# Kernel optimization log

Measured on AMD Instinct MI355X. Metric: run time of the kernel, lower is better.

## Reference

```python
import jax, jax.numpy as jnp
import numpy as np

N_AGENTS = 2
B, C, H, W = 4, 64, 200, 352


def _conv(x, w, b):
    # x: (n, Cin, H, W), w: (Cout, Cin, 3, 3), 'SAME' padding, stride 1
    y = jax.lax.conv_general_dilated(
        x, w, window_strides=(1, 1), padding='SAME',
        dimension_numbers=('NCHW', 'OIHW', 'NCHW'))
    return y + b[None, :, None, None]


def setup_inputs() -> dict:
    key = jax.random.key(0)
    ks = jax.random.split(key, 4)
    s = 0.05  # small init so sigmoid/tanh stay in useful range
    x = jax.random.normal(ks[0], (N_AGENTS, B, C, H, W), dtype=jnp.float32)
    msg_w = jax.random.normal(ks[1], (C, 2 * C, 3, 3), dtype=jnp.float32) * s
    msg_b = jnp.zeros((C,), jnp.float32)
    gates_w = jax.random.normal(ks[2], (2 * C, 3 * C, 3, 3), dtype=jnp.float32) * s
    gates_b = jnp.zeros((2 * C,), jnp.float32)
    can_w = jax.random.normal(ks[3], (C, 3 * C, 3, 3), dtype=jnp.float32) * s
    can_b = jnp.zeros((C,), jnp.float32)
    return {'x': x, 'msg_w': msg_w, 'msg_b': msg_b,
            'gates_w': gates_w, 'gates_b': gates_b,
            'can_w': can_w, 'can_b': can_b}


def reference(x, msg_w, msg_b, gates_w, gates_b, can_w, can_b):
    # num_iteration=1; only new_x[0] (agent 0's updated feature) is returned,
    # so we compute exactly that path.
    x0, x1 = x[0], x[1]                       # each (B, C, H, W)
    neighbor = jnp.concatenate([x0, x1], axis=1)   # (B, 2C, H, W)
    message = _conv(neighbor, msg_w, msg_b)        # (B, C, H, W)
    agg = 0.5 * (x0 + message)                     # 'avg' over stacked pair
    cat_feat = jnp.concatenate([x0, agg], axis=1)  # (B, 2C, H, W)

    # ConvGRU: batch_first input (1, B, 2C, H, W) -> sequence length B, batch 1
    h0 = jnp.zeros((1, C, H, W), cat_feat.dtype)

    def step(h, inp):
        inp = inp[None]                                     # (1, 2C, H, W)
        comb = jnp.concatenate([inp, h], axis=1)            # (1, 3C, H, W)
        gates = jax.nn.sigmoid(_conv(comb, gates_w, gates_b))
        reset, update = jnp.split(gates, 2, axis=1)         # each (1, C, H, W)
        comb2 = jnp.concatenate([inp, reset * h], axis=1)
        cnm = jnp.tanh(_conv(comb2, can_w, can_b))
        h_next = (1.0 - update) * h + update * cnm
        return h_next, h_next[0]

    _, out = jax.lax.scan(step, h0, cat_feat)  # out: (B, C, H, W)
    return out
```

## Files before the change

### kernel.cpp

```cpp
#include <hip/hip_runtime.h>
#include <math.h>
#include <string.h>

#define HH 200
#define WW 352
#define HWSZ (HH*WW)
#define CHW (64L*HWSZ)

enum { EPI_MSG=0, EPI_GATES=1, EPI_CAND=2 };

typedef __attribute__((ext_vector_type(8))) _Float16 f16x8;
typedef __attribute__((ext_vector_type(4))) float f32x4;
typedef __attribute__((ext_vector_type(4))) unsigned int uint4v;
typedef __attribute__((ext_vector_type(4))) unsigned short ushort4v;

__device__ __forceinline__ unsigned short f2h(float f) {
    _Float16 h = (_Float16)f;
    return __builtin_bit_cast(unsigned short, h);
}
__device__ __forceinline__ float h2f(unsigned short u) {
    return (float)__builtin_bit_cast(_Float16, u);
}

__device__ __forceinline__ void load_lds16(const unsigned short* g,
                                           unsigned short* l) {
    __builtin_amdgcn_global_load_lds(
        (const __attribute__((address_space(1))) unsigned int*)g,
        (__attribute__((address_space(3))) unsigned int*)l, 16, 0, 0);
}

__global__ void prepack_k(const float* __restrict__ mw,
                          const float* __restrict__ gw,
                          const float* __restrict__ cw,
                          unsigned short* __restrict__ pw,
                          unsigned short* __restrict__ zp)
{
    const int MSG_I = 4*18432;
    const int GAT_I = 12*18432;
    const int CAN_I = 6*18432;
    const int TOTAL = MSG_I + GAT_I + CAN_I;
    int idx = blockIdx.x*256 + threadIdx.x;
    if (idx >= TOTAL) {
        int r = idx - TOTAL;
        if (r < 128) zp[r] = 0;
        return;
    }
    const float* w; int cin, nkb, rel; unsigned short* base;
    if (idx < MSG_I)              { w=mw; cin=128; nkb=4; rel=idx;              base=pw; }
    else if (idx < MSG_I+GAT_I)   { w=gw; cin=192; nkb=6; rel=idx-MSG_I;        base=pw+73728; }
    else                          { w=cw; cin=192; nkb=6; rel=idx-MSG_I-GAT_I;  base=pw+294912; }
    int chunk = rel / 18432, r = rel - chunk*18432;
    int j = r & 7, lane = (r >> 3) & 63, cfsh = r >> 9;
    int cf = cfsh & 3, sh = cfsh >> 2;
    int q = lane >> 4, n16 = lane & 15;
    int co_l = cf*16 + n16, ch = q*8 + j;
    int cogrp = chunk / nkb, kb = chunk - cogrp*nkb;
    float f = w[(((long)(cogrp*64 + co_l))*cin + kb*32 + ch)*9 + sh];
    base[(size_t)chunk*18432 + r] = f2h(f);
}

__global__ void convert_all_k(const float* __restrict__ x,
                              unsigned short* __restrict__ xb0_all,
                              unsigned short* __restrict__ xb1_all)
{
    int idx = blockIdx.x*256 + threadIdx.x;
    int cp   = idx & 15;
    int rest = idx >> 4;
    int px4  = rest % 17600;
    int r2   = rest / 17600;
    int hb = r2 & 1, ag = (r2 >> 1) & 1, t = r2 >> 2;
    const float* src = x + ((size_t)(ag*4 + t))*CHW
                         + (size_t)(hb*32 + 2*cp)*HWSZ + (size_t)px4*4;
    float4 a = *(const float4*)src;
    float4 b = *(const float4*)(src + HWSZ);
    unsigned int* dst = (unsigned int*)((ag ? xb1_all : xb0_all)
                        + (size_t)t*CHW + (size_t)hb*HWSZ*32) + (size_t)px4*64 + cp;
    dst[0]  = (unsigned)f2h(a.x) | ((unsigned)f2h(b.x) << 16);
    dst[16] = (unsigned)f2h(a.y) | ((unsigned)f2h(b.y) << 16);
    dst[32] = (unsigned)f2h(a.z) | ((unsigned)f2h(b.z) << 16);
    dst[48] = (unsigned)f2h(a.w) | ((unsigned)f2h(b.w) << 16);
}

template<int EPI>
__global__ __launch_bounds__(256, 2)
void conv_mfma_k(const unsigned short* __restrict__ seg0b,
                 const unsigned short* __restrict__ seg1b,
                 const unsigned short* __restrict__ seg2b,
                 int nkb, int nkb_stride, int grp_base,
                 const unsigned short* __restrict__ pw,
                 const unsigned short* __restrict__ zp,
                 const float* __restrict__ bias,
                 const unsigned short* e_hb,
                 const unsigned short* __restrict__ e_updb,
                 float* out_f,
                 unsigned short* out_b,
                 unsigned short* out_b2)
{
    __shared__ unsigned short s_in0[340*32];
    __shared__ unsigned short s_in1[340*32];
    __shared__ unsigned short s_w[9*4*64*8];

    const int tid  = threadIdx.x;
    const int lane = tid & 63;
    const int wv   = tid >> 6;
    const int n16  = lane & 15;
    const int q    = lane >> 4;

    const int z = blockIdx.z;
    int grp, ts = 0;
    if (EPI == EPI_MSG) { ts = z; grp = 0; } else grp = z + grp_base;

    const unsigned short* s0 = seg0b + (EPI==EPI_MSG ? (size_t)ts*CHW : 0);
    const unsigned short* s1 = seg1b + (EPI==EPI_MSG ? (size_t)ts*CHW : 0);
    unsigned short* ob = out_b;
    if (EPI == EPI_MSG) ob = (ts < 3) ? out_b + (size_t)ts*CHW : out_b2;

    const int x0p = blockIdx.x * 32;
    const int y0  = blockIdx.y * 8;

    int hdst0 = 0, hdst1 = 0; size_t hsrc0 = 0, hsrc1 = 0;
    bool hval0 = false, hval1 = false;
    {
        auto hcalc = [&](int s, int& hdst, size_t& hsrc, bool& hval) {
            int hp = s >> 2, gs = s & 3;
            int row, col;
            if (hp < 34)      { row = 0; col = hp; }
            else if (hp < 68) { row = 9; col = hp - 34; }
            else { int k = hp - 68; row = 1 + (k >> 1); col = (k & 1) * 33; }
            int pos = row*34 + col;
            int gy = y0 + row - 1, gx = x0p + col - 1;
            hdst = (pos << 5) + (gs << 3);
            int g = (gs ^ pos ^ (pos >> 2)) & 3;
            if ((unsigned)gy < (unsigned)HH && (unsigned)gx < (unsigned)WW) {
                hval = true;
                hsrc = ((size_t)(gy*WW + gx) << 5) + (size_t)(g << 3);
            }
        };
        if (tid < 336) hcalc(tid, hdst0, hsrc0, hval0);
        if (tid < 80)  hcalc(tid + 256, hdst1, hsrc1, hval1);
    }

    auto srcof = [&](int kb) -> const unsigned short* {
        return ((kb < 2) ? s0 : (kb < 4) ? s1 : seg2b) + (size_t)(kb & 1)*HWSZ*32;
    };

    struct HV { uint4v a, b; };
    auto halo_load = [&](int kb, HV& h) {
        const unsigned short* src = srcof(kb);
        if (tid < 336) h.a = *(const uint4v*)(hval0 ? src + hsrc0 : zp);
        if (tid < 80)  h.b = *(const uint4v*)(hval1 ? src + hsrc1 : zp);
    };
    auto halo_write = [&](unsigned short* bin, const HV& h) {
        if (tid < 336) *(uint4v*)&bin[hdst0] = h.a;
        if (tid < 80)  *(uint4v*)&bin[hdst1] = h.b;
    };

    auto stage_in = [&](int kb, unsigned short* bin) {
        const unsigned short* src = srcof(kb);
#pragma unroll
        for (int j = 0; j < 4; ++j) {
            const int c    = wv + 4*j;
            const int row  = 1 + (c >> 1);
            const int colh = c & 1;
            const int gy   = y0 + row - 1;
            const int p0   = row*34 + 1 + colh*16;
            const int pl   = p0 + (lane >> 2);
            const int g    = ((lane & 3) ^ pl ^ (pl >> 2)) & 3;
            const int gx   = x0p + colh*16 + (lane >> 2);
            load_lds16(src + (((size_t)(gy*WW + gx)) << 5) + (g << 3),
                       &bin[(size_t)p0 << 5]);
        }
    };
    auto stage_w = [&](int kb) {
        const unsigned short* wsrc = pw + (size_t)(grp*nkb_stride + kb)*18432;
#pragma unroll
        for (int i = 0; i < 9; ++i) {
            const int u = wv + 4*i;
            load_lds16(wsrc + (size_t)u*512 + (size_t)lane*8, &s_w[(size_t)u*512]);
        }
    };

    f32x4 acc[4][4];
#pragma unroll
    for (int cf=0; cf<4; ++cf)
#pragma unroll
        for (int p=0; p<4; ++p) acc[cf][p] = (f32x4){0.f,0.f,0.f,0.f};

    auto compute = [&](const unsigned short* sin) {
#pragma unroll
        for (int ky = 0; ky < 3; ++ky) {
#pragma unroll
            for (int kx = 0; kx < 3; ++kx) {
                const int sh = ky*3 + kx;
                f16x8 aw[4];
#pragma unroll
                for (int cf = 0; cf < 4; ++cf)
                    aw[cf] = *(const f16x8*)&s_w[((sh*4 + cf)*64 + lane)*8];
#pragma unroll
                for (int p = 0; p < 4; ++p) {
                    const int rl = 2*wv + (p >> 1) + ky;
                    const int cl = 16*(p & 1) + n16 + kx;
                    const int pos = rl*34 + cl;
                    const int sw = (q ^ pos ^ (pos >> 2)) & 3;
                    f16x8 bfr = *(const f16x8*)&sin[(pos << 5) + (sw << 3)];
#pragma unroll
                    for (int cf = 0; cf < 4; ++cf)
                        acc[cf][p] = __builtin_amdgcn_mfma_f32_16x16x32_f16(
                                         aw[cf], bfr, acc[cf][p], 0, 0, 0);
                }
            }
        }
    };

    HV h0, h1;
    stage_in(0, s_in0);
    stage_w(0);
    halo_load(0, h0);

    for (int kb = 0; kb < nkb; kb += 2) {
        halo_write(s_in0, h0);
        __syncthreads();
        halo_load(kb + 1, h1);
        stage_in(kb + 1, s_in1);
        __builtin_amdgcn_sched_barrier(0);
        compute(s_in0);
        __syncthreads();
        stage_w(kb + 1);
        halo_write(s_in1, h1);
        __syncthreads();
        if (kb + 2 < nkb) {
            halo_load(kb + 2, h0);
            stage_in(kb + 2, s_in0);
            __builtin_amdgcn_sched_barrier(0);
        }
        compute(s_in1);
        __syncthreads();
        if (kb + 2 < nkb) stage_w(kb + 2);
    }

#pragma unroll
    for (int cf = 0; cf < 4; ++cf) {
        const int half   = cf >> 1;
        const int cobase = grp*64 + cf*16 + q*4;
        const int cmod   = (cf & 1)*16 + q*4;
#pragma unroll
        for (int p = 0; p < 4; ++p) {
            const int row = y0 + 2*wv + (p >> 1);
            const int col = x0p + 16*(p & 1) + n16;
            if (row >= HH) continue;
            const long pix = (long)row*WW + col;
            const size_t iidx = (((size_t)half*HWSZ + pix) << 5) + cmod;
            float v[4];
#pragma unroll
            for (int r = 0; r < 4; ++r) v[r] = acc[cf][p][r] + bias[cobase + r];

            if (EPI == EPI_MSG) {
                ushort4v xv = *(const ushort4v*)&s0[iidx];
                ushort4v s;
#pragma unroll
                for (int r = 0; r < 4; ++r)
                    s[r] = f2h(0.5f*(h2f(xv[r]) + v[r]));
                *(ushort4v*)&ob[iidx] = s;
            } else if (EPI == EPI_GATES) {
                if (grp == 0) {
                    ushort4v hv = e_hb ? *(const ushort4v*)&e_hb[iidx]
                                       : (ushort4v){0,0,0,0};
                    ushort4v s;
#pragma unroll
                    for (int r = 0; r < 4; ++r) {
                        float g = 1.f/(1.f + __expf(-v[r]));
                        s[r] = f2h(g * h2f(hv[r]));
                    }
                    *(ushort4v*)&out_b[iidx] = s;
                } else {
                    ushort4v s;
#pragma unroll
                    for (int r = 0; r < 4; ++r)
                        s[r] = f2h(1.f/(1.f + __expf(-v[r])));
                    *(ushort4v*)&out_b2[iidx] = s;
                }
            } else {
                ushort4v uv = *(const ushort4v*)&e_updb[iidx];
                ushort4v hv = e_hb ? *(const ushort4v*)&e_hb[iidx]
                                   : (ushort4v){0,0,0,0};
                ushort4v s;
#pragma unroll
                for (int r = 0; r < 4; ++r) {
                    float cnm = tanhf(v[r]);
                    float u   = h2f(uv[r]);
                    float hn  = (1.f - u)*h2f(hv[r]) + u*cnm;
                    out_f[(long)(cobase+r)*HWSZ + pix] = hn;
                    s[r] = f2h(hn);
                }
                *(ushort4v*)&out_b[iidx] = s;
            }
        }
    }
}

extern "C" void kernel_launch(void* const* d_in, const int* in_sizes, int n_in,
                              void* d_out, int out_size, void* d_ws, size_t ws_size,
                              hipStream_t stream)
{
    const float* x       = (const float*)d_in[0];
    const float* msg_w   = (const float*)d_in[1];
    const float* msg_b   = (const float*)d_in[2];
    const float* gates_w = (const float*)d_in[3];
    const float* gates_b = (const float*)d_in[4];
    const float* can_w   = (const float*)d_in[5];
    const float* can_b   = (const float*)d_in[6];
    float* out = (float*)d_out;

    unsigned short* W       = (unsigned short*)d_ws;
    unsigned short* xb0_all = W;
    unsigned short* aggb3   = W + 4*CHW;
    unsigned short* rhb     = W + 5*CHW;
    unsigned short* updb    = W + 6*CHW;
    unsigned short* hb      = W + 7*CHW;
    unsigned short* pw      = W + 8*CHW;
    unsigned short* pw_msg  = pw;
    unsigned short* pw_gat  = pw + 73728;
    unsigned short* pw_can  = pw + 294912;
    unsigned short* zp      = pw + 405504;

    unsigned short* outU16   = (unsigned short*)d_out;
    unsigned short* xb1_all  = outU16;
    unsigned short* aggbase  = outU16 + 4*CHW;

    prepack_k<<<dim3(1585), dim3(256), 0, stream>>>(msg_w, gates_w, can_w, pw, zp);
    convert_all_k<<<dim3(17600), dim3(256), 0, stream>>>(x, xb0_all, xb1_all);

    conv_mfma_k<EPI_MSG><<<dim3(11,25,4), dim3(256), 0, stream>>>(
        xb0_all, xb1_all, nullptr, 4, 4, 0, pw_msg, zp, msg_b,
        nullptr, nullptr, nullptr, aggbase, aggb3);

    for (int t = 0; t < 4; ++t) {
        const unsigned short* xt  = xb0_all + (size_t)t*CHW;
        const unsigned short* agt = (t < 3) ? aggbase + (size_t)t*CHW : aggb3;
        const unsigned short* hprev = t ? hb : nullptr;

        conv_mfma_k<EPI_GATES><<<dim3(11,25, t ? 2 : 1), dim3(256), 0, stream>>>(
            xt, agt, hb, t ? 6 : 4, 6, t ? 0 : 1, pw_gat, zp, gates_b,
            hprev, nullptr, nullptr, rhb, updb);
        conv_mfma_k<EPI_CAND><<<dim3(11,25,1), dim3(256), 0, stream>>>(
            xt, agt, rhb, t ? 6 : 4, 6, 0, pw_can, zp, can_b,
            hprev, updb, out + (size_t)t*CHW, hb, nullptr);
    }
}
```

Before: 428.4 us.

## Split candidate and first-step gate convs into 32-channel blocks with double-buffered weights

Adds a CF template parameter so a block can compute 32 output channels instead of 64. The candidate conv and the t=0 update-gate conv now launch twice as many blocks, which fills more CUs for these single-group launches that previously ran only 275 blocks. The CF=2 path double-buffers weight tiles in LDS, removing the weight-restage barrier. The cost is that each input tile is staged twice across channel groups, and the extra prepacked gate weights are stored in scratch space inside the output buffer.

```diff
diff --git a/kernel.cpp b/kernel.cpp
--- a/kernel.cpp
+++ b/kernel.cpp
@@ -33,30 +33,40 @@
                           const float* __restrict__ gw,
                           const float* __restrict__ cw,
                           unsigned short* __restrict__ pw,
+                          unsigned short* __restrict__ gatu,
                           unsigned short* __restrict__ zp)
 {
-    const int MSG_I = 4*18432;
-    const int GAT_I = 12*18432;
-    const int CAN_I = 6*18432;
-    const int TOTAL = MSG_I + GAT_I + CAN_I;
+    const int MSG_I  = 4*18432;
+    const int GAT_I  = 12*18432;
+    const int CAN_I  = 12*9216;
+    const int GATU_I = 12*9216;
+    const int TOTAL  = MSG_I + GAT_I + CAN_I + GATU_I;
     int idx = blockIdx.x*256 + threadIdx.x;
     if (idx >= TOTAL) {
         int r = idx - TOTAL;
         if (r < 128) zp[r] = 0;
         return;
     }
-    const float* w; int cin, nkb, rel; unsigned short* base;
-    if (idx < MSG_I)              { w=mw; cin=128; nkb=4; rel=idx;              base=pw; }
-    else if (idx < MSG_I+GAT_I)   { w=gw; cin=192; nkb=6; rel=idx-MSG_I;        base=pw+73728; }
-    else                          { w=cw; cin=192; nkb=6; rel=idx-MSG_I-GAT_I;  base=pw+294912; }
-    int chunk = rel / 18432, r = rel - chunk*18432;
+    const float* w; int cin, nkb, CF, co_off, rel; unsigned short* base;
+    if (idx < MSG_I) {
+        w=mw; cin=128; nkb=4; CF=4; co_off=0;  rel=idx;                    base=pw;
+    } else if (idx < MSG_I+GAT_I) {
+        w=gw; cin=192; nkb=6; CF=4; co_off=0;  rel=idx-MSG_I;              base=pw+73728;
+    } else if (idx < MSG_I+GAT_I+CAN_I) {
+        w=cw; cin=192; nkb=6; CF=2; co_off=0;  rel=idx-MSG_I-GAT_I;        base=pw+294912;
+    } else {
+        w=gw; cin=192; nkb=6; CF=2; co_off=64; rel=idx-MSG_I-GAT_I-CAN_I;  base=gatu;
+    }
+    int per = CF*4608;
+    int chunk = rel / per, r = rel - chunk*per;
     int j = r & 7, lane = (r >> 3) & 63, cfsh = r >> 9;
-    int cf = cfsh & 3, sh = cfsh >> 2;
+    int cf = cfsh & (CF-1), sh = cfsh / CF;
     int q = lane >> 4, n16 = lane & 15;
     int co_l = cf*16 + n16, ch = q*8 + j;
     int cogrp = chunk / nkb, kb = chunk - cogrp*nkb;
-    float f = w[(((long)(cogrp*64 + co_l))*cin + kb*32 + ch)*9 + sh];
-    base[(size_t)chunk*18432 + r] = f2h(f);
+    int co = co_off + cogrp*(CF*16) + co_l;
+    float f = w[(((long)co)*cin + kb*32 + ch)*9 + sh];
+    base[(size_t)chunk*per + r] = f2h(f);
 }
 
 __global__ void convert_all_k(const float* __restrict__ x,
@@ -81,12 +91,12 @@
     dst[48] = (unsigned)f2h(a.w) | ((unsigned)f2h(b.w) << 16);
 }
 
-template<int EPI>
+template<int EPI, int CF>
 __global__ __launch_bounds__(256, 2)
 void conv_mfma_k(const unsigned short* __restrict__ seg0b,
                  const unsigned short* __restrict__ seg1b,
                  const unsigned short* __restrict__ seg2b,
-                 int nkb, int nkb_stride, int grp_base,
+                 int nkb, int nkb_stride, int co_off,
                  const unsigned short* __restrict__ pw,
                  const unsigned short* __restrict__ zp,
                  const float* __restrict__ bias,
@@ -98,7 +108,7 @@
 {
     __shared__ unsigned short s_in0[340*32];
     __shared__ unsigned short s_in1[340*32];
-    __shared__ unsigned short s_w[9*4*64*8];
+    __shared__ unsigned short s_w[18432];
 
     const int tid  = threadIdx.x;
     const int lane = tid & 63;
@@ -108,7 +118,7 @@
 
     const int z = blockIdx.z;
     int grp, ts = 0;
-    if (EPI == EPI_MSG) { ts = z; grp = 0; } else grp = z + grp_base;
+    if (EPI == EPI_MSG) { ts = z; grp = 0; } else grp = z;
 
     const unsigned short* s0 = seg0b + (EPI==EPI_MSG ? (size_t)ts*CHW : 0);
     const unsigned short* s1 = seg1b + (EPI==EPI_MSG ? (size_t)ts*CHW : 0);
@@ -171,31 +181,33 @@
                        &bin[(size_t)p0 << 5]);
         }
     };
-    auto stage_w = [&](int kb) {
-        const unsigned short* wsrc = pw + (size_t)(grp*nkb_stride + kb)*18432;
-#pragma unroll
-        for (int i = 0; i < 9; ++i) {
+    auto stage_w = [&](int kb, unsigned short* bw) {
+        const unsigned short* wsrc = pw + (size_t)(grp*nkb_stride + kb)*(CF*4608);
+        constexpr int NCH = (CF == 4) ? 36 : 18;
+#pragma unroll
+        for (int i = 0; i < (NCH + 3) / 4; ++i) {
             const int u = wv + 4*i;
-            load_lds16(wsrc + (size_t)u*512 + (size_t)lane*8, &s_w[(size_t)u*512]);
-        }
-    };
-
-    f32x4 acc[4][4];
-#pragma unroll
-    for (int cf=0; cf<4; ++cf)
+            if (u < NCH)
+                load_lds16(wsrc + (size_t)u*512 + (size_t)lane*8, &bw[(size_t)u*512]);
+        }
+    };
+
+    f32x4 acc[CF][4];
+#pragma unroll
+    for (int cf=0; cf<CF; ++cf)
 #pragma unroll
         for (int p=0; p<4; ++p) acc[cf][p] = (f32x4){0.f,0.f,0.f,0.f};
 
-    auto compute = [&](const unsigned short* sin) {
+    auto compute = [&](const unsigned short* sin, const unsigned short* swt) {
 #pragma unroll
         for (int ky = 0; ky < 3; ++ky) {
 #pragma unroll
             for (int kx = 0; kx < 3; ++kx) {
                 const int sh = ky*3 + kx;
-                f16x8 aw[4];
-#pragma unroll
-                for (int cf = 0; cf < 4; ++cf)
-                    aw[cf] = *(const f16x8*)&s_w[((sh*4 + cf)*64 + lane)*8];
+                f16x8 aw[CF];
+#pragma unroll
+                for (int cf = 0; cf < CF; ++cf)
+                    aw[cf] = *(const f16x8*)&swt[((sh*CF + cf)*64 + lane)*8];
 #pragma unroll
                 for (int p = 0; p < 4; ++p) {
                     const int rl = 2*wv + (p >> 1) + ky;
@@ -204,7 +216,7 @@
                     const int sw = (q ^ pos ^ (pos >> 2)) & 3;
                     f16x8 bfr = *(const f16x8*)&sin[(pos << 5) + (sw << 3)];
 #pragma unroll
-                    for (int cf = 0; cf < 4; ++cf)
+                    for (int cf = 0; cf < CF; ++cf)
                         acc[cf][p] = __builtin_amdgcn_mfma_f32_16x16x32_f16(
                                          aw[cf], bfr, acc[cf][p], 0, 0, 0);
                 }
@@ -213,36 +225,55 @@
     };
 
     HV h0, h1;
-    stage_in(0, s_in0);
-    stage_w(0);
-    halo_load(0, h0);
-
-    for (int kb = 0; kb < nkb; kb += 2) {
-        halo_write(s_in0, h0);
-        __syncthreads();
-        halo_load(kb + 1, h1);
-        stage_in(kb + 1, s_in1);
-        __builtin_amdgcn_sched_barrier(0);
-        compute(s_in0);
-        __syncthreads();
-        stage_w(kb + 1);
-        halo_write(s_in1, h1);
-        __syncthreads();
-        if (kb + 2 < nkb) {
-            halo_load(kb + 2, h0);
-            stage_in(kb + 2, s_in0);
+    if constexpr (CF == 4) {
+        stage_in(0, s_in0);
+        stage_w(0, s_w);
+        halo_load(0, h0);
+        for (int kb = 0; kb < nkb; kb += 2) {
+            halo_write(s_in0, h0);
+            __syncthreads();
+            halo_load(kb + 1, h1);
+            stage_in(kb + 1, s_in1);
             __builtin_amdgcn_sched_barrier(0);
-        }
-        compute(s_in1);
-        __syncthreads();
-        if (kb + 2 < nkb) stage_w(kb + 2);
-    }
-
-#pragma unroll
-    for (int cf = 0; cf < 4; ++cf) {
-        const int half   = cf >> 1;
-        const int cobase = grp*64 + cf*16 + q*4;
-        const int cmod   = (cf & 1)*16 + q*4;
+            compute(s_in0, s_w);
+            __syncthreads();
+            stage_w(kb + 1, s_w);
+            halo_write(s_in1, h1);
+            __syncthreads();
+            if (kb + 2 < nkb) {
+                halo_load(kb + 2, h0);
+                stage_in(kb + 2, s_in0);
+                __builtin_amdgcn_sched_barrier(0);
+            }
+            compute(s_in1, s_w);
+            __syncthreads();
+            if (kb + 2 < nkb) stage_w(kb + 2, s_w);
+        }
+    } else {
+        unsigned short* s_w0 = s_w;
+        unsigned short* s_w1 = s_w + 9216;
+        stage_in(0, s_in0); stage_w(0, s_w0); halo_load(0, h0);
+        for (int kb = 0; kb < nkb; kb += 2) {
+            halo_write(s_in0, h0);
+            __syncthreads();
+            stage_in(kb + 1, s_in1); stage_w(kb + 1, s_w1); halo_load(kb + 1, h1);
+            __builtin_amdgcn_sched_barrier(0);
+            compute(s_in0, s_w0);
+            halo_write(s_in1, h1);
+            __syncthreads();
+            if (kb + 2 < nkb) {
+                stage_in(kb + 2, s_in0); stage_w(kb + 2, s_w0); halo_load(kb + 2, h0);
+                __builtin_amdgcn_sched_barrier(0);
+            }
+            compute(s_in1, s_w1);
+        }
+    }
+
+#pragma unroll
+    for (int cf = 0; cf < CF; ++cf) {
+        const int co_r0 = co_off + grp*(CF*16) + cf*16 + q*4;
+        const int half  = (co_r0 >> 5) & 1;
+        const int cmod  = co_r0 & 31;
 #pragma unroll
         for (int p = 0; p < 4; ++p) {
             const int row = y0 + 2*wv + (p >> 1);
@@ -252,7 +283,7 @@
             const size_t iidx = (((size_t)half*HWSZ + pix) << 5) + cmod;
             float v[4];
 #pragma unroll
-            for (int r = 0; r < 4; ++r) v[r] = acc[cf][p][r] + bias[cobase + r];
+            for (int r = 0; r < 4; ++r) v[r] = acc[cf][p][r] + bias[co_r0 + r];
 
             if (EPI == EPI_MSG) {
                 ushort4v xv = *(const ushort4v*)&s0[iidx];
@@ -262,7 +293,7 @@
                     s[r] = f2h(0.5f*(h2f(xv[r]) + v[r]));
                 *(ushort4v*)&ob[iidx] = s;
             } else if (EPI == EPI_GATES) {
-                if (grp == 0) {
+                if (co_r0 < 64) {
                     ushort4v hv = e_hb ? *(const ushort4v*)&e_hb[iidx]
                                        : (ushort4v){0,0,0,0};
                     ushort4v s;
@@ -273,11 +304,13 @@
                     }
                     *(ushort4v*)&out_b[iidx] = s;
                 } else {
+                    const int cu = co_r0 - 64;
+                    const size_t uidx = (((size_t)(cu >> 5)*HWSZ + pix) << 5) + (cu & 31);
                     ushort4v s;
 #pragma unroll
                     for (int r = 0; r < 4; ++r)
                         s[r] = f2h(1.f/(1.f + __expf(-v[r])));
-                    *(ushort4v*)&out_b2[iidx] = s;
+                    *(ushort4v*)&out_b2[uidx] = s;
                 }
             } else {
                 ushort4v uv = *(const ushort4v*)&e_updb[iidx];
@@ -289,7 +322,7 @@
                     float cnm = tanhf(v[r]);
                     float u   = h2f(uv[r]);
                     float hn  = (1.f - u)*h2f(hv[r]) + u*cnm;
-                    out_f[(long)(cobase+r)*HWSZ + pix] = hn;
+                    out_f[(long)(co_r0 + r)*HWSZ + pix] = hn;
                     s[r] = f2h(hn);
                 }
                 *(ushort4v*)&out_b[iidx] = s;
@@ -326,11 +359,13 @@
     unsigned short* outU16   = (unsigned short*)d_out;
     unsigned short* xb1_all  = outU16;
     unsigned short* aggbase  = outU16 + 4*CHW;
-
-    prepack_k<<<dim3(1585), dim3(256), 0, stream>>>(msg_w, gates_w, can_w, pw, zp);
+    unsigned short* pw_gatu  = outU16 + 7*CHW;
+
+    prepack_k<<<dim3(2017), dim3(256), 0, stream>>>(msg_w, gates_w, can_w,
+                                                    pw, pw_gatu, zp);
     convert_all_k<<<dim3(17600), dim3(256), 0, stream>>>(x, xb0_all, xb1_all);
 
-    conv_mfma_k<EPI_MSG><<<dim3(11,25,4), dim3(256), 0, stream>>>(
+    conv_mfma_k<EPI_MSG,4><<<dim3(11,25,4), dim3(256), 0, stream>>>(
         xb0_all, xb1_all, nullptr, 4, 4, 0, pw_msg, zp, msg_b,
         nullptr, nullptr, nullptr, aggbase, aggb3);
 
@@ -339,10 +374,16 @@
         const unsigned short* agt = (t < 3) ? aggbase + (size_t)t*CHW : aggb3;
         const unsigned short* hprev = t ? hb : nullptr;
 
-        conv_mfma_k<EPI_GATES><<<dim3(11,25, t ? 2 : 1), dim3(256), 0, stream>>>(
-            xt, agt, hb, t ? 6 : 4, 6, t ? 0 : 1, pw_gat, zp, gates_b,
-            hprev, nullptr, nullptr, rhb, updb);
-        conv_mfma_k<EPI_CAND><<<dim3(11,25,1), dim3(256), 0, stream>>>(
+        if (t == 0) {
+            conv_mfma_k<EPI_GATES,2><<<dim3(11,25,2), dim3(256), 0, stream>>>(
+                xt, agt, nullptr, 4, 6, 64, pw_gatu, zp, gates_b,
+                nullptr, nullptr, nullptr, rhb, updb);
+        } else {
+            conv_mfma_k<EPI_GATES,4><<<dim3(11,25,2), dim3(256), 0, stream>>>(
+                xt, agt, hb, 6, 6, 0, pw_gat, zp, gates_b,
+                hprev, nullptr, nullptr, rhb, updb);
+        }
+        conv_mfma_k<EPI_CAND,2><<<dim3(11,25,2), dim3(256), 0, stream>>>(
             xt, agt, rhb, t ? 6 : 4, 6, 0, pw_can, zp, can_b,
             hprev, updb, out + (size_t)t*CHW, hb, nullptr);
     }
```

Result: slower. 441.5 us (+3.0%).

## Split conv blocks into 32-output-channel halves with single-buffered LDS for occupancy

Applied to the files above, without the earlier changes.

Each conv block now computes 32 output channels instead of 64, so the grid doubles along x and the accumulator and weight tiles shrink by half. LDS input double-buffering is dropped for a single buffer with a simpler load/compute/sync loop, and launch bounds rise to allow four blocks per CU. The weight prepack layout is rewritten to match 32-channel groups. The trade-off is that each input tile is now staged twice (once per channel half), and the software pipelining that overlapped loads with MFMA work is lost in exchange for more resident waves.

```diff
diff --git a/kernel.cpp b/kernel.cpp
--- a/kernel.cpp
+++ b/kernel.cpp
@@ -35,9 +35,9 @@
                           unsigned short* __restrict__ pw,
                           unsigned short* __restrict__ zp)
 {
-    const int MSG_I = 4*18432;
-    const int GAT_I = 12*18432;
-    const int CAN_I = 6*18432;
+    const int MSG_I = 8*9216;
+    const int GAT_I = 24*9216;
+    const int CAN_I = 12*9216;
     const int TOTAL = MSG_I + GAT_I + CAN_I;
     int idx = blockIdx.x*256 + threadIdx.x;
     if (idx >= TOTAL) {
@@ -46,17 +46,17 @@
         return;
     }
     const float* w; int cin, nkb, rel; unsigned short* base;
-    if (idx < MSG_I)              { w=mw; cin=128; nkb=4; rel=idx;              base=pw; }
-    else if (idx < MSG_I+GAT_I)   { w=gw; cin=192; nkb=6; rel=idx-MSG_I;        base=pw+73728; }
-    else                          { w=cw; cin=192; nkb=6; rel=idx-MSG_I-GAT_I;  base=pw+294912; }
-    int chunk = rel / 18432, r = rel - chunk*18432;
+    if (idx < MSG_I)              { w=mw; cin=128; nkb=4; rel=idx;             base=pw; }
+    else if (idx < MSG_I+GAT_I)   { w=gw; cin=192; nkb=6; rel=idx-MSG_I;       base=pw+73728; }
+    else                          { w=cw; cin=192; nkb=6; rel=idx-MSG_I-GAT_I; base=pw+294912; }
+    int chunk = rel / 9216, r = rel - chunk*9216;
     int j = r & 7, lane = (r >> 3) & 63, cfsh = r >> 9;
-    int cf = cfsh & 3, sh = cfsh >> 2;
+    int cf = cfsh & 1, sh = cfsh >> 1;
     int q = lane >> 4, n16 = lane & 15;
     int co_l = cf*16 + n16, ch = q*8 + j;
     int cogrp = chunk / nkb, kb = chunk - cogrp*nkb;
-    float f = w[(((long)(cogrp*64 + co_l))*cin + kb*32 + ch)*9 + sh];
-    base[(size_t)chunk*18432 + r] = f2h(f);
+    float f = w[(((long)(cogrp*32 + co_l))*cin + kb*32 + ch)*9 + sh];
+    base[(size_t)chunk*9216 + r] = f2h(f);
 }
 
 __global__ void convert_all_k(const float* __restrict__ x,
@@ -82,7 +82,7 @@
 }
 
 template<int EPI>
-__global__ __launch_bounds__(256, 2)
+__global__ __launch_bounds__(256, 4)
 void conv_mfma_k(const unsigned short* __restrict__ seg0b,
                  const unsigned short* __restrict__ seg1b,
                  const unsigned short* __restrict__ seg2b,
@@ -96,9 +96,8 @@
                  unsigned short* out_b,
                  unsigned short* out_b2)
 {
-    __shared__ unsigned short s_in0[340*32];
-    __shared__ unsigned short s_in1[340*32];
-    __shared__ unsigned short s_w[9*4*64*8];
+    __shared__ unsigned short s_in[340*32];
+    __shared__ unsigned short s_w[9*2*64*8];
 
     const int tid  = threadIdx.x;
     const int lane = tid & 63;
@@ -106,16 +105,16 @@
     const int n16  = lane & 15;
     const int q    = lane >> 4;
 
-    const int z = blockIdx.z;
     int grp, ts = 0;
-    if (EPI == EPI_MSG) { ts = z; grp = 0; } else grp = z + grp_base;
+    if (EPI == EPI_MSG) { ts = blockIdx.z; grp = blockIdx.x & 1; }
+    else                { grp = (blockIdx.x & 1) + 2*blockIdx.z + grp_base; }
 
     const unsigned short* s0 = seg0b + (EPI==EPI_MSG ? (size_t)ts*CHW : 0);
     const unsigned short* s1 = seg1b + (EPI==EPI_MSG ? (size_t)ts*CHW : 0);
     unsigned short* ob = out_b;
     if (EPI == EPI_MSG) ob = (ts < 3) ? out_b + (size_t)ts*CHW : out_b2;
 
-    const int x0p = blockIdx.x * 32;
+    const int x0p = (blockIdx.x >> 1) * 32;
     const int y0  = blockIdx.y * 8;
 
     int hdst0 = 0, hdst1 = 0; size_t hsrc0 = 0, hsrc1 = 0;
@@ -150,12 +149,12 @@
         if (tid < 336) h.a = *(const uint4v*)(hval0 ? src + hsrc0 : zp);
         if (tid < 80)  h.b = *(const uint4v*)(hval1 ? src + hsrc1 : zp);
     };
-    auto halo_write = [&](unsigned short* bin, const HV& h) {
-        if (tid < 336) *(uint4v*)&bin[hdst0] = h.a;
-        if (tid < 80)  *(uint4v*)&bin[hdst1] = h.b;
-    };
-
-    auto stage_in = [&](int kb, unsigned short* bin) {
+    auto halo_write = [&](const HV& h) {
+        if (tid < 336) *(uint4v*)&s_in[hdst0] = h.a;
+        if (tid < 80)  *(uint4v*)&s_in[hdst1] = h.b;
+    };
+
+    auto stage_in = [&](int kb) {
         const unsigned short* src = srcof(kb);
 #pragma unroll
         for (int j = 0; j < 4; ++j) {
@@ -168,81 +167,68 @@
             const int g    = ((lane & 3) ^ pl ^ (pl >> 2)) & 3;
             const int gx   = x0p + colh*16 + (lane >> 2);
             load_lds16(src + (((size_t)(gy*WW + gx)) << 5) + (g << 3),
-                       &bin[(size_t)p0 << 5]);
+                       &s_in[(size_t)p0 << 5]);
         }
     };
     auto stage_w = [&](int kb) {
-        const unsigned short* wsrc = pw + (size_t)(grp*nkb_stride + kb)*18432;
-#pragma unroll
-        for (int i = 0; i < 9; ++i) {
+        const unsigned short* wsrc = pw + (size_t)(grp*nkb_stride + kb)*9216;
+#pragma unroll
+        for (int i = 0; i < 5; ++i) {
             const int u = wv + 4*i;
-            load_lds16(wsrc + (size_t)u*512 + (size_t)lane*8, &s_w[(size_t)u*512]);
-        }
-    };
-
-    f32x4 acc[4][4];
-#pragma unroll
-    for (int cf=0; cf<4; ++cf)
+            if (u < 18)
+                load_lds16(wsrc + (size_t)u*512 + (size_t)lane*8, &s_w[(size_t)u*512]);
+        }
+    };
+
+    f32x4 acc[2][4];
+#pragma unroll
+    for (int cf=0; cf<2; ++cf)
 #pragma unroll
         for (int p=0; p<4; ++p) acc[cf][p] = (f32x4){0.f,0.f,0.f,0.f};
 
-    auto compute = [&](const unsigned short* sin) {
+    auto compute = [&]() {
 #pragma unroll
         for (int ky = 0; ky < 3; ++ky) {
 #pragma unroll
             for (int kx = 0; kx < 3; ++kx) {
                 const int sh = ky*3 + kx;
-                f16x8 aw[4];
-#pragma unroll
-                for (int cf = 0; cf < 4; ++cf)
-                    aw[cf] = *(const f16x8*)&s_w[((sh*4 + cf)*64 + lane)*8];
+                f16x8 aw0 = *(const f16x8*)&s_w[((sh*2 + 0)*64 + lane)*8];
+                f16x8 aw1 = *(const f16x8*)&s_w[((sh*2 + 1)*64 + lane)*8];
 #pragma unroll
                 for (int p = 0; p < 4; ++p) {
                     const int rl = 2*wv + (p >> 1) + ky;
                     const int cl = 16*(p & 1) + n16 + kx;
                     const int pos = rl*34 + cl;
                     const int sw = (q ^ pos ^ (pos >> 2)) & 3;
-                    f16x8 bfr = *(const f16x8*)&sin[(pos << 5) + (sw << 3)];
-#pragma unroll
-                    for (int cf = 0; cf < 4; ++cf)
-                        acc[cf][p] = __builtin_amdgcn_mfma_f32_16x16x32_f16(
-                                         aw[cf], bfr, acc[cf][p], 0, 0, 0);
+                    f16x8 bfr = *(const f16x8*)&s_in[(pos << 5) + (sw << 3)];
+                    acc[0][p] = __builtin_amdgcn_mfma_f32_16x16x32_f16(aw0, bfr, acc[0][p], 0, 0, 0);
+                    acc[1][p] = __builtin_amdgcn_mfma_f32_16x16x32_f16(aw1, bfr, acc[1][p], 0, 0, 0);
                 }
             }
         }
     };
 
-    HV h0, h1;
-    stage_in(0, s_in0);
-    stage_w(0);
-    halo_load(0, h0);
-
-    for (int kb = 0; kb < nkb; kb += 2) {
-        halo_write(s_in0, h0);
+    HV h;
+    stage_in(0); stage_w(0); halo_load(0, h);
+    halo_write(h);
+    __syncthreads();
+
+    for (int kb = 0; kb < nkb; ++kb) {
+        if (kb + 1 < nkb) halo_load(kb + 1, h);
+        compute();
         __syncthreads();
-        halo_load(kb + 1, h1);
-        stage_in(kb + 1, s_in1);
-        __builtin_amdgcn_sched_barrier(0);
-        compute(s_in0);
-        __syncthreads();
-        stage_w(kb + 1);
-        halo_write(s_in1, h1);
-        __syncthreads();
-        if (kb + 2 < nkb) {
-            halo_load(kb + 2, h0);
-            stage_in(kb + 2, s_in0);
-            __builtin_amdgcn_sched_barrier(0);
-        }
-        compute(s_in1);
-        __syncthreads();
-        if (kb + 2 < nkb) stage_w(kb + 2);
-    }
-
-#pragma unroll
-    for (int cf = 0; cf < 4; ++cf) {
-        const int half   = cf >> 1;
-        const int cobase = grp*64 + cf*16 + q*4;
-        const int cmod   = (cf & 1)*16 + q*4;
+        if (kb + 1 < nkb) {
+            stage_in(kb + 1); stage_w(kb + 1);
+            halo_write(h);
+            __syncthreads();
+        }
+    }
+
+#pragma unroll
+    for (int cf = 0; cf < 2; ++cf) {
+        const int co_r0 = grp*32 + cf*16 + q*4;
+        const int half  = (co_r0 >> 5) & 1;
+        const int cmod  = co_r0 & 31;
 #pragma unroll
         for (int p = 0; p < 4; ++p) {
             const int row = y0 + 2*wv + (p >> 1);
@@ -252,7 +238,7 @@
             const size_t iidx = (((size_t)half*HWSZ + pix) << 5) + cmod;
             float v[4];
 #pragma unroll
-            for (int r = 0; r < 4; ++r) v[r] = acc[cf][p][r] + bias[cobase + r];
+            for (int r = 0; r < 4; ++r) v[r] = acc[cf][p][r] + bias[co_r0 + r];
 
             if (EPI == EPI_MSG) {
                 ushort4v xv = *(const ushort4v*)&s0[iidx];
@@ -262,7 +248,7 @@
                     s[r] = f2h(0.5f*(h2f(xv[r]) + v[r]));
                 *(ushort4v*)&ob[iidx] = s;
             } else if (EPI == EPI_GATES) {
-                if (grp == 0) {
+                if (co_r0 < 64) {
                     ushort4v hv = e_hb ? *(const ushort4v*)&e_hb[iidx]
                                        : (ushort4v){0,0,0,0};
                     ushort4v s;
@@ -273,11 +259,13 @@
                     }
                     *(ushort4v*)&out_b[iidx] = s;
                 } else {
+                    const int cu = co_r0 - 64;
+                    const size_t uidx = (((size_t)(cu >> 5)*HWSZ + pix) << 5) + (cu & 31);
                     ushort4v s;
 #pragma unroll
                     for (int r = 0; r < 4; ++r)
                         s[r] = f2h(1.f/(1.f + __expf(-v[r])));
-                    *(ushort4v*)&out_b2[iidx] = s;
+                    *(ushort4v*)&out_b2[uidx] = s;
                 }
             } else {
                 ushort4v uv = *(const ushort4v*)&e_updb[iidx];
@@ -289,7 +277,7 @@
                     float cnm = tanhf(v[r]);
                     float u   = h2f(uv[r]);
                     float hn  = (1.f - u)*h2f(hv[r]) + u*cnm;
-                    out_f[(long)(cobase+r)*HWSZ + pix] = hn;
+                    out_f[(long)(co_r0 + r)*HWSZ + pix] = hn;
                     s[r] = f2h(hn);
                 }
                 *(ushort4v*)&out_b[iidx] = s;
@@ -330,7 +318,7 @@
     prepack_k<<<dim3(1585), dim3(256), 0, stream>>>(msg_w, gates_w, can_w, pw, zp);
     convert_all_k<<<dim3(17600), dim3(256), 0, stream>>>(x, xb0_all, xb1_all);
 
-    conv_mfma_k<EPI_MSG><<<dim3(11,25,4), dim3(256), 0, stream>>>(
+    conv_mfma_k<EPI_MSG><<<dim3(22,25,4), dim3(256), 0, stream>>>(
         xb0_all, xb1_all, nullptr, 4, 4, 0, pw_msg, zp, msg_b,
         nullptr, nullptr, nullptr, aggbase, aggb3);
 
@@ -339,10 +327,16 @@
         const unsigned short* agt = (t < 3) ? aggbase + (size_t)t*CHW : aggb3;
         const unsigned short* hprev = t ? hb : nullptr;
 
-        conv_mfma_k<EPI_GATES><<<dim3(11,25, t ? 2 : 1), dim3(256), 0, stream>>>(
-            xt, agt, hb, t ? 6 : 4, 6, t ? 0 : 1, pw_gat, zp, gates_b,
-            hprev, nullptr, nullptr, rhb, updb);
-        conv_mfma_k<EPI_CAND><<<dim3(11,25,1), dim3(256), 0, stream>>>(
+        if (t == 0) {
+            conv_mfma_k<EPI_GATES><<<dim3(22,25,1), dim3(256), 0, stream>>>(
+                xt, agt, nullptr, 4, 6, 2, pw_gat, zp, gates_b,
+                nullptr, nullptr, nullptr, rhb, updb);
+        } else {
+            conv_mfma_k<EPI_GATES><<<dim3(22,25,2), dim3(256), 0, stream>>>(
+                xt, agt, hb, 6, 6, 0, pw_gat, zp, gates_b,
+                hprev, nullptr, nullptr, rhb, updb);
+        }
+        conv_mfma_k<EPI_CAND><<<dim3(22,25,1), dim3(256), 0, stream>>>(
             xt, agt, rhb, t ? 6 : 4, 6, 0, pw_can, zp, can_b,
             hprev, updb, out + (size_t)t*CHW, hb, nullptr);
     }
```

After: 422.7 us. About the same (-1.3%).
